# Optimization experiments

Measured on AMD Instinct MI355X. Metric: run time of the kernel, lower is better.

## Reference

```python
import jax, jax.numpy as jnp
import numpy as np


def setup_inputs() -> dict:
    key = jax.random.key(0)
    k1, k2, k3, k4 = jax.random.split(key, 4)
    B, C, H, W = 8, 64, 64, 64
    K = C // 8
    x = jax.random.normal(k1, (B, C, H, W), dtype=jnp.float32)
    # 1x1 conv weights (no bias): stored as [out_ch, in_ch]
    Wf = jax.random.normal(k2, (K, C), dtype=jnp.float32) * 0.05
    Wg = jax.random.normal(k3, (K, C), dtype=jnp.float32) * 0.05
    Wh = jax.random.normal(k4, (C, C), dtype=jnp.float32) * 0.05
    # gamma initialized to zero in the module; use a nonzero value so the
    # attention path contributes to the output (and gradients) in testing.
    gamma = jnp.array([0.5], dtype=jnp.float32)
    return {"x": x, "Wf": Wf, "Wg": Wg, "Wh": Wh, "gamma": gamma}


def reference(x, Wf, Wg, Wh, gamma):
    B, C, H, W = x.shape
    N = H * W
    xf = x.reshape(B, C, N)                       # [B, C, N]
    f = jnp.einsum('kc,bcn->bkn', Wf, xf)         # [B, C//8, N]
    g = jnp.einsum('kc,bcn->bkn', Wg, xf)         # [B, C//8, N]
    h = jnp.einsum('oc,bcn->bon', Wh, xf)         # [B, C, N]
    # beta[b, i, j] = f[b,:,i] . g[b,:,j]  (unscaled attention logits)
    beta = jnp.einsum('bki,bkj->bij', f, g)       # [B, N, N]
    beta = jax.nn.softmax(beta, axis=-1)
    # res[b, c, i] = sum_j h[b, c, j] * beta[b, i, j]
    res = jnp.einsum('bcj,bij->bci', h, beta)     # [B, C, N]
    res = res.reshape(B, C, H, W)
    return gamma * res + x
```

## Files before the change

kernel.cpp:

```cpp
#include <hip/hip_runtime.h>

typedef float f32x4 __attribute__((ext_vector_type(4)));
typedef float f32x16 __attribute__((ext_vector_type(16)));
typedef short s16x8 __attribute__((ext_vector_type(8)));
typedef short s16x4 __attribute__((ext_vector_type(4)));
typedef unsigned short u16;

#define NB 8
#define NC 64
#define NN 4096

__device__ __forceinline__ u16 f2bf_rne(float f) {
    unsigned u = __float_as_uint(f);
    u += 0x7FFFu + ((u >> 16) & 1u);
    return (u16)(u >> 16);
}
__device__ __forceinline__ float bf2f(u16 v) {
    return __uint_as_float(((unsigned)v) << 16);
}
__device__ __forceinline__ unsigned cvt_pk_bf16(float lo, float hi) {
    unsigned r;
    asm("v_cvt_pk_bf16_f32 %0, %1, %2" : "=v"(r) : "v"(lo), "v"(hi));
    return r;
}
__device__ __forceinline__ void pl32_swap(unsigned &a, unsigned &b) {
    asm("v_permlane32_swap_b32 %0, %1" : "+v"(a), "+v"(b));
}
__device__ __forceinline__ float exp2_hw(float x) {
    return __builtin_amdgcn_exp2f(x);
}

#define Z16 ((f32x16){0.f,0.f,0.f,0.f,0.f,0.f,0.f,0.f,0.f,0.f,0.f,0.f,0.f,0.f,0.f,0.f})

__global__ __launch_bounds__(256, 4)
void precompute_qgh(const float* __restrict__ x,
                    const float* __restrict__ Wf,
                    const float* __restrict__ Wg,
                    const float* __restrict__ Wh,
                    u16* __restrict__ Qw, u16* __restrict__ Gw,
                    u16* __restrict__ Hf)
{
    const int b  = blockIdx.x;
    const int n0 = blockIdx.y * 64;
    const int t  = threadIdx.x;
    const int wave = t >> 6, lane = t & 63, col = lane & 15, quad = lane >> 4;
    const float* xb = x + (size_t)b * NC * NN;

    __shared__ __align__(16) u16 WL[80][72];
    __shared__ __align__(16) u16 XT[64][72];

    #pragma unroll
    for (int r5 = 0; r5 < 5; r5++) {
        int v = r5 * 256 + t;
        int m = v >> 4, ks = (v & 15) << 2;
        const float* src = (m < 64) ? (Wh + m * 64 + ks)
                         : (m < 72) ? (Wf + (m - 64) * 64 + ks)
                                    : (Wg + (m - 72) * 64 + ks);
        const float scl = (m >= 64 && m < 72) ? 1.44269504088896f : 1.0f;
        f32x4 wv = *(const f32x4*)src;
        *(unsigned*)&WL[m][ks]     = (unsigned)f2bf_rne(wv[0] * scl) | ((unsigned)f2bf_rne(wv[1] * scl) << 16);
        *(unsigned*)&WL[m][ks + 2] = (unsigned)f2bf_rne(wv[2] * scl) | ((unsigned)f2bf_rne(wv[3] * scl) << 16);
    }
    #pragma unroll
    for (int r4 = 0; r4 < 4; r4++) {
        int v = r4 * 256 + t;
        int c = v >> 4, ns = (v & 15) << 2;
        f32x4 xv = *(const f32x4*)(xb + (size_t)c * NN + n0 + ns);
        #pragma unroll
        for (int e = 0; e < 4; e++) XT[ns + e][c] = f2bf_rne(xv[e]);
    }
    __syncthreads();

    const int n = n0 + wave * 16 + col;
    s16x8 bfrag[2], afrag[5][2];
    #pragma unroll
    for (int s = 0; s < 2; s++)
        bfrag[s] = *(const s16x8*)&XT[wave * 16 + col][s * 32 + quad * 8];
    #pragma unroll
    for (int mt = 0; mt < 5; mt++)
        #pragma unroll
        for (int s = 0; s < 2; s++)
            afrag[mt][s] = *(const s16x8*)&WL[mt * 16 + col][s * 32 + quad * 8];

    f32x4 d[5];
    #pragma unroll
    for (int mt = 0; mt < 5; mt++) d[mt] = (f32x4){0.f, 0.f, 0.f, 0.f};
    #pragma unroll
    for (int s = 0; s < 2; s++)
        #pragma unroll
        for (int mt = 0; mt < 5; mt++)
            d[mt] = __builtin_amdgcn_mfma_f32_16x16x32_bf16(afrag[mt][s], bfrag[s], d[mt], 0, 0, 0);

    union { s16x4 v; u16 e[4]; } pk4;
    #pragma unroll
    for (int r = 0; r < 4; r++) pk4.e[r] = f2bf_rne(d[4][r]);
    u16* qgbase = (quad < 2 ? Qw : Gw) + ((size_t)b * NN + n) * 16;
    *(s16x4*)(qgbase + (quad & 1) * 4) = pk4.v;
    if ((quad & 1) == 0) {
        s16x8 z;
        #pragma unroll
        for (int q = 0; q < 8; q++) ((u16*)&z)[q] = 0;
        *(s16x8*)(qgbase + 8) = z;
    }

    __syncthreads();
    u16 (*Hl)[72] = WL;
    #pragma unroll
    for (int mt = 0; mt < 4; mt++)
        #pragma unroll
        for (int r = 0; r < 4; r++)
            Hl[mt * 16 + quad * 4 + r][wave * 16 + col] = f2bf_rne(d[mt][r]);
    __syncthreads();

    u16* HfB = Hf + (size_t)b * NC * NN + (size_t)blockIdx.y * 4096;
    #pragma unroll
    for (int it = 0; it < 2; it++) {
        int u = it * 256 + t;
        int s_local = u >> 7, chalf = (u >> 6) & 1, l = u & 63;
        s16x8 vv = *(const s16x8*)&Hl[chalf * 32 + (l & 31)][s_local * 16 + (l >> 5) * 8];
        *(s16x8*)(HfB + (size_t)((s_local * 2 + chalf) * 512 + l * 8)) = vv;
    }
}

__global__ __launch_bounds__(256, 2)
void attention_fused(const u16* __restrict__ Qw, const u16* __restrict__ Gw,
                     const u16* __restrict__ Hf,
                     const float* __restrict__ x, const float* __restrict__ gamma,
                     float* __restrict__ out)
{
    const int b  = blockIdx.x;
    const int i0 = blockIdx.y * 64;
    const int t  = threadIdx.x;
    const int wave = t >> 6, lane = t & 63, col = lane & 31, hi = lane >> 5;

    __shared__ __align__(16) float R0a[64][36];
    __shared__ __align__(16) float R1a[64][36];
    __shared__ __align__(16) float R0b[64][36];
    __shared__ __align__(16) float R1b[64][36];
    __shared__ float Ls[2][4][32];
    __shared__ float Sc[2][32];

    const u16* Qb  = Qw + (size_t)b * NN * 16;
    const u16* Gb  = Gw + (size_t)b * NN * 16;
    const u16* Hfb = Hf + (size_t)b * NC * NN;

    const float g = gamma[0];

    s16x8 qf0 = *(const s16x8*)(Qb + (size_t)(i0 + col) * 16 + hi * 8);
    s16x8 qf1 = *(const s16x8*)(Qb + (size_t)(i0 + 32 + col) * 16 + hi * 8);

    f32x16 oacc[2][2];
    oacc[0][0] = Z16; oacc[0][1] = Z16; oacc[1][0] = Z16; oacc[1][1] = Z16;
    float ls0a = 0.f, ls0b = 0.f, ls1a = 0.f, ls1b = 0.f;

    const int jbase = wave * 1024;
    const u16* pv = Hfb + (size_t)(jbase >> 4) * 1024 + (size_t)lane * 8;

    s16x8 ga  = *(const s16x8*)(Gb + (size_t)(jbase + col) * 16 + hi * 8);
    s16x8 va0 = *(const s16x8*)(pv);
    s16x8 va1 = *(const s16x8*)(pv + 512);
    s16x8 va2 = *(const s16x8*)(pv + 1024);
    s16x8 va3 = *(const s16x8*)(pv + 1536);
    pv += 2048;

    for (int cc = 0; cc < 32; cc++) {
        s16x8 gan = *(const s16x8*)(Gb + (size_t)(jbase + cc * 32 + 32 + col) * 16 + hi * 8);
        s16x8 vn0 = *(const s16x8*)(pv);
        s16x8 vn1 = *(const s16x8*)(pv + 512);
        s16x8 vn2 = *(const s16x8*)(pv + 1024);
        s16x8 vn3 = *(const s16x8*)(pv + 1536);
        pv += 2048;

        f32x16 S0 = __builtin_amdgcn_mfma_f32_32x32x16_bf16(ga, qf0, Z16, 0, 0, 0);
        f32x16 S1 = __builtin_amdgcn_mfma_f32_32x32x16_bf16(ga, qf1, Z16, 0, 0, 0);
        #pragma unroll
        for (int r = 0; r < 16; r++) S0[r] = exp2_hw(S0[r]);
        #pragma unroll
        for (int r = 0; r < 16; r++) S1[r] = exp2_hw(S1[r]);
        #pragma unroll
        for (int r = 0; r < 16; r += 2) {
            ls0a += S0[r]; ls0b += S0[r + 1];
            ls1a += S1[r]; ls1b += S1[r + 1];
        }

        #pragma unroll
        for (int s2 = 0; s2 < 2; s2++) {
            unsigned a0 = cvt_pk_bf16(S0[8*s2+0], S0[8*s2+1]);
            unsigned a2 = cvt_pk_bf16(S0[8*s2+4], S0[8*s2+5]);
            unsigned a1 = cvt_pk_bf16(S0[8*s2+2], S0[8*s2+3]);
            unsigned a3 = cvt_pk_bf16(S0[8*s2+6], S0[8*s2+7]);
            pl32_swap(a0, a2);
            pl32_swap(a1, a3);
            union { s16x8 v; unsigned u[4]; } p0;
            p0.u[0] = a0; p0.u[1] = a1; p0.u[2] = a2; p0.u[3] = a3;
            unsigned b0 = cvt_pk_bf16(S1[8*s2+0], S1[8*s2+1]);
            unsigned b2 = cvt_pk_bf16(S1[8*s2+4], S1[8*s2+5]);
            unsigned b1 = cvt_pk_bf16(S1[8*s2+2], S1[8*s2+3]);
            unsigned b3 = cvt_pk_bf16(S1[8*s2+6], S1[8*s2+7]);
            pl32_swap(b0, b2);
            pl32_swap(b1, b3);
            union { s16x8 v; unsigned u[4]; } p1;
            p1.u[0] = b0; p1.u[1] = b1; p1.u[2] = b2; p1.u[3] = b3;
            oacc[0][0] = __builtin_amdgcn_mfma_f32_32x32x16_bf16(p0.v, s2 ? va2 : va0, oacc[0][0], 0, 0, 0);
            oacc[0][1] = __builtin_amdgcn_mfma_f32_32x32x16_bf16(p0.v, s2 ? va3 : va1, oacc[0][1], 0, 0, 0);
            oacc[1][0] = __builtin_amdgcn_mfma_f32_32x32x16_bf16(p1.v, s2 ? va2 : va0, oacc[1][0], 0, 0, 0);
            oacc[1][1] = __builtin_amdgcn_mfma_f32_32x32x16_bf16(p1.v, s2 ? va3 : va1, oacc[1][1], 0, 0, 0);
        }
        ga = gan; va0 = vn0; va1 = vn1; va2 = vn2; va3 = vn3;
    }

    float lsum0 = ls0a + ls0b;
    float lsum1 = ls1a + ls1b;
    {
        unsigned a = __float_as_uint(lsum0), c2 = a;
        pl32_swap(a, c2);
        lsum0 = __uint_as_float(a) + __uint_as_float(c2);
        unsigned d = __float_as_uint(lsum1), e2 = d;
        pl32_swap(d, e2);
        lsum1 = __uint_as_float(d) + __uint_as_float(e2);
    }

    if (hi == 0) { Ls[0][wave][col] = lsum0; Ls[1][wave][col] = lsum1; }
    if (wave & 1) {
        float (*Ra)[36] = (wave == 1) ? R0a : R1a;
        float (*Rb)[36] = (wave == 1) ? R0b : R1b;
        #pragma unroll
        for (int ch = 0; ch < 2; ch++)
            #pragma unroll
            for (int r = 0; r < 16; r++) {
                int ii = (r & 3) + 8 * (r >> 2) + 4 * hi;
                Ra[ch * 32 + col][ii] = oacc[0][ch][r];
                Rb[ch * 32 + col][ii] = oacc[1][ch][r];
            }
    }
    __syncthreads();
    if (!(wave & 1)) {
        float (*Ra)[36] = (wave == 0) ? R0a : R1a;
        float (*Rb)[36] = (wave == 0) ? R0b : R1b;
        #pragma unroll
        for (int ch = 0; ch < 2; ch++)
            #pragma unroll
            for (int r = 0; r < 16; r++) {
                int ii = (r & 3) + 8 * (r >> 2) + 4 * hi;
                oacc[0][ch][r] += Ra[ch * 32 + col][ii];
                oacc[1][ch][r] += Rb[ch * 32 + col][ii];
            }
    }
    if (wave == 1 && hi == 0)
        Sc[0][col] = g / (Ls[0][0][col] + Ls[0][1][col] + Ls[0][2][col] + Ls[0][3][col]);
    if (wave == 3 && hi == 0)
        Sc[1][col] = g / (Ls[1][0][col] + Ls[1][1][col] + Ls[1][2][col] + Ls[1][3][col]);
    if (wave == 2) {
        #pragma unroll
        for (int ch = 0; ch < 2; ch++)
            #pragma unroll
            for (int r = 0; r < 16; r++) {
                int ii = (r & 3) + 8 * (r >> 2) + 4 * hi;
                R1a[ch * 32 + col][ii] = oacc[0][ch][r];
                R1b[ch * 32 + col][ii] = oacc[1][ch][r];
            }
    }
    __syncthreads();
    if (wave == 0) {
        #pragma unroll
        for (int ch = 0; ch < 2; ch++)
            #pragma unroll
            for (int r = 0; r < 16; r++) {
                int ii = (r & 3) + 8 * (r >> 2) + 4 * hi;
                R0a[ch * 32 + col][ii] = oacc[0][ch][r] + R1a[ch * 32 + col][ii];
                R0b[ch * 32 + col][ii] = oacc[1][ch][r] + R1b[ch * 32 + col][ii];
            }
    }
    __syncthreads();

    const int oc = t >> 2, q = t & 3;
    float (*slab)[36] = (q < 2) ? R0a : R0b;
    const float* sc = Sc[q >> 1];
    const float* xr = x   + ((size_t)b * NC + oc) * NN + i0;
    float*    orow  = out + ((size_t)b * NC + oc) * NN + i0;
    #pragma unroll
    for (int e = 0; e < 4; e++) {
        const int il = q * 16 + e * 4;
        const int ii = (q & 1) * 16 + e * 4;
        f32x4 o = *(const f32x4*)&slab[oc][ii];
        f32x4 xv = *(const f32x4*)(xr + il);
        f32x4 rv;
        #pragma unroll
        for (int k = 0; k < 4; k++) rv[k] = o[k] * sc[ii + k] + xv[k];
        *(f32x4*)(orow + il) = rv;
    }
}

extern "C" void kernel_launch(void* const* d_in, const int* in_sizes, int n_in,
                              void* d_out, int out_size, void* d_ws, size_t ws_size,
                              hipStream_t stream) {
    const float* x     = (const float*)d_in[0];
    const float* Wf    = (const float*)d_in[1];
    const float* Wg    = (const float*)d_in[2];
    const float* Wh    = (const float*)d_in[3];
    const float* gamma = (const float*)d_in[4];
    float* out = (float*)d_out;

    u16* Hf = (u16*)d_ws;
    u16* Gw = Hf + (size_t)NB * NC * NN;
    u16* Qw = Gw + (size_t)NB * NN * 16;

    precompute_qgh<<<dim3(NB, 64), 256, 0, stream>>>(x, Wf, Wg, Wh, Qw, Gw, Hf);
    attention_fused<<<dim3(NB, 64), 256, 0, stream>>>(Qw, Gw, Hf, x, gamma, out);
}
```

Measured before the change: 99.37 us.

## Software-pipeline QK MFMA and prefetch two chunks ahead in attention loop

```diff
diff --git a/kernel.cpp b/kernel.cpp
--- a/kernel.cpp
+++ b/kernel.cpp
@@ -99,7 +99,7 @@
     if ((quad & 1) == 0) {
         s16x8 z;
         #pragma unroll
-        for (int q = 0; q < 8; q++) ((u16*)&z)[q] = 0;
+        for (int qz = 0; qz < 8; qz++) ((u16*)&z)[qz] = 0;
         *(s16x8*)(qgbase + 8) = z;
     }
 
@@ -154,59 +154,72 @@
     float ls0a = 0.f, ls0b = 0.f, ls1a = 0.f, ls1b = 0.f;
 
     const int jbase = wave * 1024;
-    const u16* pv = Hfb + (size_t)(jbase >> 4) * 1024 + (size_t)lane * 8;
-
-    s16x8 ga  = *(const s16x8*)(Gb + (size_t)(jbase + col) * 16 + hi * 8);
-    s16x8 va0 = *(const s16x8*)(pv);
-    s16x8 va1 = *(const s16x8*)(pv + 512);
-    s16x8 va2 = *(const s16x8*)(pv + 1024);
-    s16x8 va3 = *(const s16x8*)(pv + 1536);
-    pv += 2048;
+    const u16* pvb = Hfb + (size_t)(jbase >> 4) * 1024 + (size_t)lane * 8;
+    const u16* gb0 = Gb + (size_t)(jbase + col) * 16 + hi * 8;
+
+    s16x8 gaA = *(const s16x8*)(gb0);
+    s16x8 vA0 = *(const s16x8*)(pvb);
+    s16x8 vA1 = *(const s16x8*)(pvb + 512);
+    s16x8 vA2 = *(const s16x8*)(pvb + 1024);
+    s16x8 vA3 = *(const s16x8*)(pvb + 1536);
+    s16x8 gaB = *(const s16x8*)(gb0 + 512);
+    s16x8 vB0 = *(const s16x8*)(pvb + 2048);
+    s16x8 vB1 = *(const s16x8*)(pvb + 2048 + 512);
+    s16x8 vB2 = *(const s16x8*)(pvb + 2048 + 1024);
+    s16x8 vB3 = *(const s16x8*)(pvb + 2048 + 1536);
+
+    f32x16 S0c = __builtin_amdgcn_mfma_f32_32x32x16_bf16(gaA, qf0, Z16, 0, 0, 0);
+    f32x16 S1c = __builtin_amdgcn_mfma_f32_32x32x16_bf16(gaA, qf1, Z16, 0, 0, 0);
 
     for (int cc = 0; cc < 32; cc++) {
-        s16x8 gan = *(const s16x8*)(Gb + (size_t)(jbase + cc * 32 + 32 + col) * 16 + hi * 8);
-        s16x8 vn0 = *(const s16x8*)(pv);
-        s16x8 vn1 = *(const s16x8*)(pv + 512);
-        s16x8 vn2 = *(const s16x8*)(pv + 1024);
-        s16x8 vn3 = *(const s16x8*)(pv + 1536);
-        pv += 2048;
-
-        f32x16 S0 = __builtin_amdgcn_mfma_f32_32x32x16_bf16(ga, qf0, Z16, 0, 0, 0);
-        f32x16 S1 = __builtin_amdgcn_mfma_f32_32x32x16_bf16(ga, qf1, Z16, 0, 0, 0);
-        #pragma unroll
-        for (int r = 0; r < 16; r++) S0[r] = exp2_hw(S0[r]);
-        #pragma unroll
-        for (int r = 0; r < 16; r++) S1[r] = exp2_hw(S1[r]);
-        #pragma unroll
-        for (int r = 0; r < 16; r += 2) {
-            ls0a += S0[r]; ls0b += S0[r + 1];
-            ls1a += S1[r]; ls1b += S1[r + 1];
-        }
+        #pragma unroll
+        for (int r = 0; r < 16; r++) S0c[r] = exp2_hw(S0c[r]);
+        #pragma unroll
+        for (int r = 0; r < 16; r++) S1c[r] = exp2_hw(S1c[r]);
+
+        f32x16 T0 = __builtin_amdgcn_mfma_f32_32x32x16_bf16(gaB, qf0, Z16, 0, 0, 0);
+        f32x16 T1 = __builtin_amdgcn_mfma_f32_32x32x16_bf16(gaB, qf1, Z16, 0, 0, 0);
 
         #pragma unroll
         for (int s2 = 0; s2 < 2; s2++) {
-            unsigned a0 = cvt_pk_bf16(S0[8*s2+0], S0[8*s2+1]);
-            unsigned a2 = cvt_pk_bf16(S0[8*s2+4], S0[8*s2+5]);
-            unsigned a1 = cvt_pk_bf16(S0[8*s2+2], S0[8*s2+3]);
-            unsigned a3 = cvt_pk_bf16(S0[8*s2+6], S0[8*s2+7]);
+            unsigned a0 = cvt_pk_bf16(S0c[8*s2+0], S0c[8*s2+1]);
+            unsigned a2 = cvt_pk_bf16(S0c[8*s2+4], S0c[8*s2+5]);
+            unsigned a1 = cvt_pk_bf16(S0c[8*s2+2], S0c[8*s2+3]);
+            unsigned a3 = cvt_pk_bf16(S0c[8*s2+6], S0c[8*s2+7]);
             pl32_swap(a0, a2);
             pl32_swap(a1, a3);
             union { s16x8 v; unsigned u[4]; } p0;
             p0.u[0] = a0; p0.u[1] = a1; p0.u[2] = a2; p0.u[3] = a3;
-            unsigned b0 = cvt_pk_bf16(S1[8*s2+0], S1[8*s2+1]);
-            unsigned b2 = cvt_pk_bf16(S1[8*s2+4], S1[8*s2+5]);
-            unsigned b1 = cvt_pk_bf16(S1[8*s2+2], S1[8*s2+3]);
-            unsigned b3 = cvt_pk_bf16(S1[8*s2+6], S1[8*s2+7]);
+            unsigned b0 = cvt_pk_bf16(S1c[8*s2+0], S1c[8*s2+1]);
+            unsigned b2 = cvt_pk_bf16(S1c[8*s2+4], S1c[8*s2+5]);
+            unsigned b1 = cvt_pk_bf16(S1c[8*s2+2], S1c[8*s2+3]);
+            unsigned b3 = cvt_pk_bf16(S1c[8*s2+6], S1c[8*s2+7]);
             pl32_swap(b0, b2);
             pl32_swap(b1, b3);
             union { s16x8 v; unsigned u[4]; } p1;
             p1.u[0] = b0; p1.u[1] = b1; p1.u[2] = b2; p1.u[3] = b3;
-            oacc[0][0] = __builtin_amdgcn_mfma_f32_32x32x16_bf16(p0.v, s2 ? va2 : va0, oacc[0][0], 0, 0, 0);
-            oacc[0][1] = __builtin_amdgcn_mfma_f32_32x32x16_bf16(p0.v, s2 ? va3 : va1, oacc[0][1], 0, 0, 0);
-            oacc[1][0] = __builtin_amdgcn_mfma_f32_32x32x16_bf16(p1.v, s2 ? va2 : va0, oacc[1][0], 0, 0, 0);
-            oacc[1][1] = __builtin_amdgcn_mfma_f32_32x32x16_bf16(p1.v, s2 ? va3 : va1, oacc[1][1], 0, 0, 0);
+            oacc[0][0] = __builtin_amdgcn_mfma_f32_32x32x16_bf16(p0.v, s2 ? vA2 : vA0, oacc[0][0], 0, 0, 0);
+            oacc[0][1] = __builtin_amdgcn_mfma_f32_32x32x16_bf16(p0.v, s2 ? vA3 : vA1, oacc[0][1], 0, 0, 0);
+            oacc[1][0] = __builtin_amdgcn_mfma_f32_32x32x16_bf16(p1.v, s2 ? vA2 : vA0, oacc[1][0], 0, 0, 0);
+            oacc[1][1] = __builtin_amdgcn_mfma_f32_32x32x16_bf16(p1.v, s2 ? vA3 : vA1, oacc[1][1], 0, 0, 0);
         }
-        ga = gan; va0 = vn0; va1 = vn1; va2 = vn2; va3 = vn3;
+
+        #pragma unroll
+        for (int r = 0; r < 16; r += 2) {
+            ls0a += S0c[r]; ls0b += S0c[r + 1];
+            ls1a += S1c[r]; ls1b += S1c[r + 1];
+        }
+
+        gaA = gaB; vA0 = vB0; vA1 = vB1; vA2 = vB2; vA3 = vB3;
+        {
+            const u16* np = pvb + (size_t)(cc + 2) * 2048;
+            gaB = *(const s16x8*)(gb0 + (size_t)(cc + 2) * 512);
+            vB0 = *(const s16x8*)(np);
+            vB1 = *(const s16x8*)(np + 512);
+            vB2 = *(const s16x8*)(np + 1024);
+            vB3 = *(const s16x8*)(np + 1536);
+        }
+        S0c = T0; S1c = T1;
     }
 
     float lsum0 = ls0a + ls0b;
```

Measured after the change: 101.6 us. 2.2% more time.
